# Performance work log

Measured on AMD Instinct MI355X. Metric: run time of the kernel, lower is better.

The kernel has to match this reference:

```python
import jax, jax.numpy as jnp
import numpy as np


def setup_inputs() -> dict:
    key = jax.random.key(0)
    k1, k2, k3 = jax.random.split(key, 3)
    shape = (16, 128, 128, 64)  # [B, H, W, C]
    return {
        "query": jax.random.normal(k1, shape, dtype=jnp.float32),
        "keys": jax.random.normal(k2, shape, dtype=jnp.float32),
        "values": jax.random.normal(k3, shape, dtype=jnp.float32),
    }


def reference(query, keys, values):
    # Attention over channel dim C, feature dim = H*W.
    # scores[b, q, k] = sum_{h,w} Q[b,h,w,q] * K[b,h,w,k]
    scores = jnp.einsum("bhwq,bhwk->bqk", query, keys)
    attn = jax.nn.softmax(scores, axis=-1)  # softmax over keys k
    # out[b,h,w,q] = sum_k attn[b,q,k] * V[b,h,w,k]
    out = jnp.einsum("bqk,bhwk->bhwq", attn, values)
    return out
```

## Files before the change

### kernel.cpp

```cpp
#include <hip/hip_runtime.h>


#define S_SPLIT 32
#define CHUNK (16384 / S_SPLIT)
#define TILE_ROWS 32

__global__ __launch_bounds__(256) void scores_kernel(
    const float* __restrict__ Q, const float* __restrict__ K,
    float* __restrict__ partial) {
  const int bs = blockIdx.x;
  const int b = bs / S_SPLIT;
  const int s = bs % S_SPLIT;
  const int tid = threadIdx.x;
  const int w = tid >> 6;
  const int l = tid & 63;
  const int q0 = (l >> 3) * 8;
  const int k0 = (l & 7) * 8;

  __shared__ union {
    struct { float4 q[TILE_ROWS * 16]; float4 k[TILE_ROWS * 16]; } t;
    float red[2][4096];
  } lds;

  float acc[8][8];
#pragma unroll
  for (int i = 0; i < 8; ++i)
#pragma unroll
    for (int j = 0; j < 8; ++j) acc[i][j] = 0.f;

  const float4* Qg = (const float4*)(Q + ((size_t)b * 16384 + (size_t)s * CHUNK) * 64);
  const float4* Kg = (const float4*)(K + ((size_t)b * 16384 + (size_t)s * CHUNK) * 64);

  for (int t = 0; t < CHUNK / TILE_ROWS; ++t) {
    __syncthreads();
    lds.t.q[tid]       = Qg[t * 512 + tid];
    lds.t.q[tid + 256] = Qg[t * 512 + tid + 256];
    lds.t.k[tid]       = Kg[t * 512 + tid];
    lds.t.k[tid + 256] = Kg[t * 512 + tid + 256];
    __syncthreads();

#pragma unroll
    for (int i = 0; i < 8; ++i) {
      const int r = (i << 2) + w;
      float4 qa = lds.t.q[r * 16 + (q0 >> 2)];
      float4 qb = lds.t.q[r * 16 + (q0 >> 2) + 1];
      float4 ka = lds.t.k[r * 16 + (k0 >> 2)];
      float4 kb = lds.t.k[r * 16 + (k0 >> 2) + 1];
      float qv[8] = {qa.x, qa.y, qa.z, qa.w, qb.x, qb.y, qb.z, qb.w};
      float kv[8] = {ka.x, ka.y, ka.z, ka.w, kb.x, kb.y, kb.z, kb.w};
#pragma unroll
      for (int ii = 0; ii < 8; ++ii)
#pragma unroll
        for (int jj = 0; jj < 8; ++jj)
          acc[ii][jj] += qv[ii] * kv[jj];
    }
  }

  __syncthreads();
  if (w >= 2) {
    float4* dst = (float4*)lds.red[w - 2];
#pragma unroll
    for (int i = 0; i < 8; ++i) {
      dst[(q0 + i) * 16 + (k0 >> 2)]     = make_float4(acc[i][0], acc[i][1], acc[i][2], acc[i][3]);
      dst[(q0 + i) * 16 + (k0 >> 2) + 1] = make_float4(acc[i][4], acc[i][5], acc[i][6], acc[i][7]);
    }
  }
  __syncthreads();
  if (w < 2) {
    float4* dst = (float4*)lds.red[w];
#pragma unroll
    for (int i = 0; i < 8; ++i) {
      float4 u = dst[(q0 + i) * 16 + (k0 >> 2)];
      float4 v = dst[(q0 + i) * 16 + (k0 >> 2) + 1];
      dst[(q0 + i) * 16 + (k0 >> 2)]     = make_float4(u.x + acc[i][0], u.y + acc[i][1], u.z + acc[i][2], u.w + acc[i][3]);
      dst[(q0 + i) * 16 + (k0 >> 2) + 1] = make_float4(v.x + acc[i][4], v.y + acc[i][5], v.z + acc[i][6], v.w + acc[i][7]);
    }
  }
  __syncthreads();
  float4* p4 = (float4*)(partial + (size_t)bs * 4096);
  const float4* r0 = (const float4*)lds.red[0];
  const float4* r1 = (const float4*)lds.red[1];
#pragma unroll
  for (int c = 0; c < 4; ++c) {
    float4 x = r0[c * 256 + tid];
    float4 y = r1[c * 256 + tid];
    p4[c * 256 + tid] = make_float4(x.x + y.x, x.y + y.y, x.z + y.z, x.w + y.w);
  }
}

__global__ __launch_bounds__(64) void softmax_kernel(
    const float* __restrict__ partial, float* __restrict__ attn) {
  const int bq = blockIdx.x;
  const int b = bq >> 6;
  const int q = bq & 63;
  const int k = threadIdx.x;

  float v = 0.f;
  for (int s = 0; s < S_SPLIT; ++s)
    v += partial[((size_t)(b * S_SPLIT + s) * 64 + q) * 64 + k];

  float m = v;
#pragma unroll
  for (int off = 32; off > 0; off >>= 1)
    m = fmaxf(m, __shfl_xor(m, off, 64));
  float e = __expf(v - m);
  float sum = e;
#pragma unroll
  for (int off = 32; off > 0; off >>= 1)
    sum += __shfl_xor(sum, off, 64);
  attn[(size_t)bq * 64 + k] = e / sum;
}

__global__ __launch_bounds__(256) void out_kernel(
    const float* __restrict__ V, const float* __restrict__ attn,
    float* __restrict__ out) {
  const int blk = blockIdx.x;
  const int b = blk >> 8;
  const int tile = blk & 255;
  const int tid = threadIdx.x;
  const int w = tid >> 6;
  const int l = tid & 63;

  __shared__ float4 ldsV[64 * 16];

  float a[64];
  const float4* arow = (const float4*)(attn + ((size_t)b * 64 + l) * 64);
#pragma unroll
  for (int j = 0; j < 16; ++j) {
    float4 t = arow[j];
    a[4 * j]     = t.x;
    a[4 * j + 1] = t.y;
    a[4 * j + 2] = t.z;
    a[4 * j + 3] = t.w;
  }

  const float4* Vg = (const float4*)(V + ((size_t)b * 16384 + (size_t)tile * 64) * 64);
#pragma unroll
  for (int c = 0; c < 4; ++c)
    ldsV[c * 256 + tid] = Vg[c * 256 + tid];
  __syncthreads();

  float* outg = out + ((size_t)b * 16384 + (size_t)tile * 64) * 64;
  for (int i = 0; i < 16; ++i) {
    const int r = w * 16 + i;
    float acc = 0.f;
#pragma unroll
    for (int j = 0; j < 16; ++j) {
      float4 v = ldsV[r * 16 + j];
      acc += a[4 * j] * v.x + a[4 * j + 1] * v.y + a[4 * j + 2] * v.z + a[4 * j + 3] * v.w;
    }
    outg[(size_t)r * 64 + l] = acc;
  }
}

extern "C" void kernel_launch(void* const* d_in, const int* in_sizes, int n_in,
                              void* d_out, int out_size, void* d_ws, size_t ws_size,
                              hipStream_t stream) {
  const float* Q = (const float*)d_in[0];
  const float* K = (const float*)d_in[1];
  const float* V = (const float*)d_in[2];
  float* out = (float*)d_out;

  float* partial = (float*)d_ws;
  float* attn = partial + (size_t)16 * S_SPLIT * 4096;

  scores_kernel<<<16 * S_SPLIT, 256, 0, stream>>>(Q, K, partial);
  softmax_kernel<<<16 * 64, 64, 0, stream>>>(partial, attn);
  out_kernel<<<16 * 256, 256, 0, stream>>>(V, attn, out);
}
```

Baseline: 264.0 us.

## Double-buffer scores tiles with async LDS loads; stream V directly in out kernel

The scores kernel now stages Q/K tiles into two LDS buffers using global_load_lds direct-to-LDS copies. The next tile is prefetched while the current one is computed, and one barrier per tile is removed. The out kernel drops its LDS staging of V: each wave walks 64 contiguous rows and reads V with wave-uniform global loads, using four partial accumulators. This also cuts the grid to a quarter of the blocks. Correctness relies on the barrier waiting on the outstanding LDS DMA. The direct V reads depend on cache broadcast efficiency, and fewer blocks may lower parallelism.

```diff
diff --git a/kernel.cpp b/kernel.cpp
--- a/kernel.cpp
+++ b/kernel.cpp
@@ -4,6 +4,7 @@
 #define S_SPLIT 32
 #define CHUNK (16384 / S_SPLIT)
 #define TILE_ROWS 32
+#define NTILES (CHUNK / TILE_ROWS)
 
 __global__ __launch_bounds__(256) void scores_kernel(
     const float* __restrict__ Q, const float* __restrict__ K,
@@ -18,7 +19,7 @@
   const int k0 = (l & 7) * 8;
 
   __shared__ union {
-    struct { float4 q[TILE_ROWS * 16]; float4 k[TILE_ROWS * 16]; } t;
+    struct { float4 q[2][512]; float4 k[2][512]; } t;
     float red[2][4096];
   } lds;
 
@@ -28,24 +29,40 @@
 #pragma unroll
     for (int j = 0; j < 8; ++j) acc[i][j] = 0.f;
 
-  const float4* Qg = (const float4*)(Q + ((size_t)b * 16384 + (size_t)s * CHUNK) * 64);
-  const float4* Kg = (const float4*)(K + ((size_t)b * 16384 + (size_t)s * CHUNK) * 64);
+  const char* Qg = (const char*)(Q + ((size_t)b * 16384 + (size_t)s * CHUNK) * 64);
+  const char* Kg = (const char*)(K + ((size_t)b * 16384 + (size_t)s * CHUNK) * 64);
 
-  for (int t = 0; t < CHUNK / TILE_ROWS; ++t) {
+  auto stage = [&](int t, int p) {
+    const char* qsrc = Qg + (size_t)t * 8192;
+    const char* ksrc = Kg + (size_t)t * 8192;
+    char* qdst = (char*)&lds.t.q[p][0];
+    char* kdst = (char*)&lds.t.k[p][0];
+#pragma unroll
+    for (int c = 0; c < 2; ++c) {
+      const int m = w + c * 4;
+      __builtin_amdgcn_global_load_lds(
+          (const __attribute__((address_space(1))) unsigned*)(qsrc + m * 1024 + l * 16),
+          (__attribute__((address_space(3))) unsigned*)(qdst + m * 1024), 16, 0, 0);
+      __builtin_amdgcn_global_load_lds(
+          (const __attribute__((address_space(1))) unsigned*)(ksrc + m * 1024 + l * 16),
+          (__attribute__((address_space(3))) unsigned*)(kdst + m * 1024), 16, 0, 0);
+    }
+  };
+
+  stage(0, 0);
+  for (int t = 0; t < NTILES; ++t) {
     __syncthreads();
-    lds.t.q[tid]       = Qg[t * 512 + tid];
-    lds.t.q[tid + 256] = Qg[t * 512 + tid + 256];
-    lds.t.k[tid]       = Kg[t * 512 + tid];
-    lds.t.k[tid + 256] = Kg[t * 512 + tid + 256];
-    __syncthreads();
+    if (t + 1 < NTILES) stage(t + 1, (t + 1) & 1);
+    const float4* bq = lds.t.q[t & 1];
+    const float4* bk = lds.t.k[t & 1];
 
 #pragma unroll
     for (int i = 0; i < 8; ++i) {
       const int r = (i << 2) + w;
-      float4 qa = lds.t.q[r * 16 + (q0 >> 2)];
-      float4 qb = lds.t.q[r * 16 + (q0 >> 2) + 1];
-      float4 ka = lds.t.k[r * 16 + (k0 >> 2)];
-      float4 kb = lds.t.k[r * 16 + (k0 >> 2) + 1];
+      float4 qa = bq[r * 16 + (q0 >> 2)];
+      float4 qb = bq[r * 16 + (q0 >> 2) + 1];
+      float4 ka = bk[r * 16 + (k0 >> 2)];
+      float4 kb = bk[r * 16 + (k0 >> 2) + 1];
       float qv[8] = {qa.x, qa.y, qa.z, qa.w, qb.x, qb.y, qb.z, qb.w};
       float kv[8] = {ka.x, ka.y, ka.z, ka.w, kb.x, kb.y, kb.z, kb.w};
 #pragma unroll
@@ -115,13 +132,10 @@
     const float* __restrict__ V, const float* __restrict__ attn,
     float* __restrict__ out) {
   const int blk = blockIdx.x;
-  const int b = blk >> 8;
-  const int tile = blk & 255;
-  const int tid = threadIdx.x;
-  const int w = tid >> 6;
-  const int l = tid & 63;
-
-  __shared__ float4 ldsV[64 * 16];
+  const int b = blk >> 6;
+  const int tile = blk & 63;
+  const int w = threadIdx.x >> 6;
+  const int l = threadIdx.x & 63;
 
   float a[64];
   const float4* arow = (const float4*)(attn + ((size_t)b * 64 + l) * 64);
@@ -134,22 +148,26 @@
     a[4 * j + 3] = t.w;
   }
 
-  const float4* Vg = (const float4*)(V + ((size_t)b * 16384 + (size_t)tile * 64) * 64);
+  const int row0 = tile * 256 + w * 64;
+  const float4* Vg = (const float4*)(V + ((size_t)b * 16384 + row0) * 64);
+  float* outg = out + ((size_t)b * 16384 + row0) * 64;
+
+#pragma unroll 2
+  for (int r = 0; r < 64; ++r) {
+    const float4* vrow = Vg + r * 16;
+    float acc0 = 0.f, acc1 = 0.f, acc2 = 0.f, acc3 = 0.f;
 #pragma unroll
-  for (int c = 0; c < 4; ++c)
-    ldsV[c * 256 + tid] = Vg[c * 256 + tid];
-  __syncthreads();
-
-  float* outg = out + ((size_t)b * 16384 + (size_t)tile * 64) * 64;
-  for (int i = 0; i < 16; ++i) {
-    const int r = w * 16 + i;
-    float acc = 0.f;
-#pragma unroll
-    for (int j = 0; j < 16; ++j) {
-      float4 v = ldsV[r * 16 + j];
-      acc += a[4 * j] * v.x + a[4 * j + 1] * v.y + a[4 * j + 2] * v.z + a[4 * j + 3] * v.w;
+    for (int j = 0; j < 16; j += 4) {
+      float4 v0 = vrow[j];
+      float4 v1 = vrow[j + 1];
+      float4 v2 = vrow[j + 2];
+      float4 v3 = vrow[j + 3];
+      acc0 += a[4*j+ 0] * v0.x + a[4*j+ 1] * v0.y + a[4*j+ 2] * v0.z + a[4*j+ 3] * v0.w;
+      acc1 += a[4*j+ 4] * v1.x + a[4*j+ 5] * v1.y + a[4*j+ 6] * v1.z + a[4*j+ 7] * v1.w;
+      acc2 += a[4*j+ 8] * v2.x + a[4*j+ 9] * v2.y + a[4*j+10] * v2.z + a[4*j+11] * v2.w;
+      acc3 += a[4*j+12] * v3.x + a[4*j+13] * v3.y + a[4*j+14] * v3.z + a[4*j+15] * v3.w;
     }
-    outg[(size_t)r * 64 + l] = acc;
+    outg[(size_t)r * 64 + l] = (acc0 + acc1) + (acc2 + acc3);
   }
 }
 
@@ -166,5 +184,5 @@
 
   scores_kernel<<<16 * S_SPLIT, 256, 0, stream>>>(Q, K, partial);
   softmax_kernel<<<16 * 64, 64, 0, stream>>>(partial, attn);
-  out_kernel<<<16 * 256, 256, 0, stream>>>(V, attn, out);
+  out_kernel<<<16 * 64, 256, 0, stream>>>(V, attn, out);
 }
```

Measured after the change: 490.8 us. 85.9% more time.
